# Kernel tuning notes

Measured on AMD Instinct MI355X. Metric: run time of the kernel, lower is better.

Reference implementation:

```python
import jax, jax.numpy as jnp
import numpy as np
from jax.ops import segment_sum

N_NODES = 50000
N_EDGES = 50000
N_GRAPHS = 1024


def _inv_deg(idx, num_segments):
    deg = segment_sum(jnp.ones(idx.shape[0], jnp.float32), idx, num_segments=num_segments)
    return jnp.where(deg > 0, 1.0 / deg, 0.0)


def hypergraph_conv(x, W, b, node_idx, edge_idx):
    # PyG HypergraphConv (use_attention=False, heads=1, hyperedge_weight=1):
    # out = D^{-1} H B^{-1} H^T (X W) + b
    D = _inv_deg(node_idx, N_NODES)   # inverse node degree [N]
    B = _inv_deg(edge_idx, N_EDGES)   # inverse hyperedge degree [E]
    xl = x @ W                         # [N, out]
    # node -> hyperedge aggregation
    edge_feat = B[:, None] * segment_sum(xl[node_idx], edge_idx, num_segments=N_EDGES)
    # hyperedge -> node aggregation
    out = D[:, None] * segment_sum(edge_feat[edge_idx], node_idx, num_segments=N_NODES)
    return out + b


def global_mean_pool(x, batch):
    s = segment_sum(x, batch, num_segments=N_GRAPHS)
    cnt = segment_sum(jnp.ones(x.shape[0], jnp.float32), batch, num_segments=N_GRAPHS)
    return s / jnp.maximum(cnt, 1.0)[:, None]


def setup_inputs() -> dict:
    key = jax.random.key(0)
    ks = jax.random.split(key, 16)
    F, H = 128, 256
    def lin(k, fi, fo):
        s = 1.0 / np.sqrt(fi)
        k1, k2 = jax.random.split(k)
        return (jax.random.uniform(k1, (fi, fo), jnp.float32, -s, s),
                jax.random.uniform(k2, (fo,), jnp.float32, -s, s))
    W1, b1 = lin(ks[0], F, H)
    W2, b2 = lin(ks[1], H, 2 * H)
    W3, b3 = lin(ks[2], 2 * H, H)
    Wl1, bl1 = lin(ks[3], H, H // 2)
    Wl2, bl2 = lin(ks[4], H // 2, 1)
    x = jax.random.normal(ks[5], (N_NODES, F), jnp.float32)
    hyperedge_index = jax.random.randint(ks[6], (2, 400000), 0, N_EDGES, jnp.int64)
    batch = jnp.sort(jax.random.randint(ks[7], (N_NODES,), 0, N_GRAPHS, jnp.int64))
    return {"x": x, "hyperedge_index": hyperedge_index, "batch": batch,
            "W1": W1, "b1": b1, "W2": W2, "b2": b2, "W3": W3, "b3": b3,
            "Wl1": Wl1, "bl1": bl1, "Wl2": Wl2, "bl2": bl2}


def reference(x, hyperedge_index, batch, W1, b1, W2, b2, W3, b3, Wl1, bl1, Wl2, bl2):
    node_idx, edge_idx = hyperedge_index[0], hyperedge_index[1]
    h = jax.nn.relu(hypergraph_conv(x, W1, b1, node_idx, edge_idx))
    h = jax.nn.relu(hypergraph_conv(h, W2, b2, node_idx, edge_idx))
    h = jax.nn.relu(hypergraph_conv(h, W3, b3, node_idx, edge_idx))
    g = global_mean_pool(h, batch)              # [G, H]
    g = jax.nn.relu(g @ Wl1 + bl1)
    out = g @ Wl2 + bl2                          # [G, 1]
    return out
```

## Files before the change

kernel.cpp:

```cpp
#include <hip/hip_runtime.h>
#include <hip/hip_bf16.h>

#define N_NODES  50000
#define N_EDGES  50000
#define N_INC    400000
#define N_GRAPHS 1024
#define M_PAD    50048
#define SEG_CAP  50176

typedef __bf16 bf16x8 __attribute__((ext_vector_type(8)));
typedef float  f32x4  __attribute__((ext_vector_type(4)));

__device__ __forceinline__ unsigned short f2bf(float f) {
    __hip_bfloat16 h = __float2bfloat16(f);
    return __builtin_bit_cast(unsigned short, h);
}
__device__ __forceinline__ float bflo(unsigned int u) {
    return __builtin_bit_cast(float, u << 16);
}
__device__ __forceinline__ float bfhi(unsigned int u) {
    return __builtin_bit_cast(float, u & 0xffff0000u);
}
__device__ __forceinline__ unsigned int packbf(float a, float b) {
    return (unsigned int)f2bf(a) | ((unsigned int)f2bf(b) << 16);
}
__device__ __forceinline__ void load_lds16(const unsigned short* g, unsigned short* l) {
    __builtin_amdgcn_global_load_lds((const __attribute__((address_space(1))) void*)g,
                                     (__attribute__((address_space(3))) void*)l, 16, 0, 0);
}

__global__ __launch_bounds__(256) void normhist_kernel(const int* __restrict__ hei,
                                                       const int* __restrict__ braw,
                                                       int* __restrict__ nidx, int* __restrict__ eidx,
                                                       unsigned short* __restrict__ rn,
                                                       unsigned short* __restrict__ re,
                                                       int* __restrict__ ndeg, int* __restrict__ edeg,
                                                       int* __restrict__ gcnt,
                                                       int* __restrict__ goff_src) {
    __shared__ int s32;
    int t = threadIdx.x;
    if (t == 0) s32 = 0;
    __syncthreads();
    int probe = hei[4 * t + 1] | hei[4 * t + 3];
    if (probe) s32 = 1;
    __syncthreads();
    int is32 = s32;
    int i = blockIdx.x * 256 + t;
    if (i < N_INC) {
        int n, e;
        if (is32) { n = hei[i];     e = hei[N_INC + i]; }
        else      { n = hei[2 * i]; e = hei[2 * N_INC + 2 * i]; }
        nidx[i] = n; eidx[i] = e;
        rn[i] = (unsigned short)atomicAdd(&ndeg[n], 1);
        re[i] = (unsigned short)atomicAdd(&edeg[e], 1);
    }
    if (i < N_NODES) {
        int b = is32 ? braw[i] : braw[2 * i];
        (void)goff_src;
        atomicAdd(&gcnt[b], 1);
    }
}

__global__ __launch_bounds__(256) void scan_up_f(const int* __restrict__ edeg,
                                                 const int* __restrict__ ndeg,
                                                 const int* __restrict__ gcnt,
                                                 int* __restrict__ eoff, int* __restrict__ noff,
                                                 int* __restrict__ goff,
                                                 int* __restrict__ partials) {
    __shared__ int lds[256];
    int b = blockIdx.x, t = threadIdx.x;
    const int* in; int* outp; int lb;
    if (b < 49)      { in = edeg; outp = eoff; lb = b; }
    else if (b < 98) { in = ndeg; outp = noff; lb = b - 49; }
    else             { in = gcnt; outp = goff; lb = 0; }
    int base = lb * 1024 + t * 4;
    int4 v = *(const int4*)(in + base);
    int s = v.x + v.y + v.z + v.w;
    lds[t] = s;
    __syncthreads();
    for (int off = 1; off < 256; off <<= 1) {
        int u = (t >= off) ? lds[t - off] : 0;
        __syncthreads();
        lds[t] += u;
        __syncthreads();
    }
    int excl = lds[t] - s;
    if (t == 255) partials[b] = lds[255];
    int4 o;
    o.x = excl;
    o.y = excl + v.x;
    o.z = o.y + v.y;
    o.w = o.z + v.z;
    *(int4*)(outp + base) = o;
}

__global__ __launch_bounds__(128) void scan_mid_f(int* __restrict__ partials) {
    __shared__ int lds[99];
    int t = threadIdx.x;
    if (t < 99) lds[t] = partials[t];
    __syncthreads();
    if (t < 3) {
        int lo = (t == 0) ? 0 : (t == 1 ? 49 : 98);
        int hi = (t == 0) ? 49 : (t == 1 ? 98 : 99);
        int run = 0;
        for (int i = lo; i < hi; ++i) { int x = lds[i]; lds[i] = run; run += x; }
    }
    __syncthreads();
    if (t < 99) partials[t] = lds[t];
}

__global__ __launch_bounds__(256) void scan_down_f(int* __restrict__ eoff,
                                                   int* __restrict__ noff,
                                                   int* __restrict__ goff,
                                                   const int* __restrict__ partials) {
    int b = blockIdx.x, t = threadIdx.x;
    int* outp; int lb;
    if (b < 49)      { outp = eoff; lb = b; }
    else if (b < 98) { outp = noff; lb = b - 49; }
    else             { outp = goff; lb = 0; }
    int base = lb * 1024 + t * 4;
    int p = partials[b];
    int4 v = *(const int4*)(outp + base);
    v.x += p; v.y += p; v.z += p; v.w += p;
    *(int4*)(outp + base) = v;
}

#define NB_CSR  1563
#define NB_CONV 6250
#define NB_W1   128
#define NB_W2   512
#define NB_W3   512
__global__ __launch_bounds__(256) void prep_kernel(const int* __restrict__ nidx,
                                                   const int* __restrict__ eidx,
                                                   const unsigned short* __restrict__ rn,
                                                   const unsigned short* __restrict__ re,
                                                   const int* __restrict__ eoff,
                                                   const int* __restrict__ noff,
                                                   unsigned short* __restrict__ csre,
                                                   unsigned short* __restrict__ csrn,
                                                   const float* __restrict__ x,
                                                   unsigned short* __restrict__ xbf,
                                                   const float* __restrict__ W1, unsigned short* __restrict__ wt1,
                                                   const float* __restrict__ W2, unsigned short* __restrict__ wt2,
                                                   const float* __restrict__ W3, unsigned short* __restrict__ wt3) {
    int b = blockIdx.x, t = threadIdx.x;
    if (b < NB_CSR) {
        int i = b * 256 + t;
        if (i < N_INC) {
            int n = nidx[i], e = eidx[i];
            csre[eoff[e] + re[i]] = (unsigned short)n;
            csrn[noff[n] + rn[i]] = (unsigned short)e;
        }
    } else if (b < NB_CSR + NB_CONV) {
        int i = (b - NB_CSR) * 256 + t;
        float4 v = *(const float4*)(x + 4 * (size_t)i);
        ushort4 o;
        o.x = f2bf(v.x); o.y = f2bf(v.y); o.z = f2bf(v.z); o.w = f2bf(v.w);
        *(ushort4*)(xbf + 4 * (size_t)i) = o;
    } else if (b < NB_CSR + NB_CONV + NB_W1) {
        int i = (b - NB_CSR - NB_CONV) * 256 + t;
        int k = i >> 8, n = i & 255;
        wt1[n * 128 + k] = f2bf(W1[i]);
    } else if (b < NB_CSR + NB_CONV + NB_W1 + NB_W2) {
        int i = (b - NB_CSR - NB_CONV - NB_W1) * 256 + t;
        int k = i >> 9, n = i & 511;
        wt2[n * 256 + k] = f2bf(W2[i]);
    } else {
        int i = (b - NB_CSR - NB_CONV - NB_W1 - NB_W2) * 256 + t;
        int k = i >> 8, n = i & 255;
        wt3[n * 512 + k] = f2bf(W3[i]);
    }
}

template <bool EPI>
__global__ __launch_bounds__(256) void gemm128_kernel(const unsigned short* __restrict__ A,
                                                      const unsigned short* __restrict__ Bt,
                                                      const float* __restrict__ bias,
                                                      unsigned short* __restrict__ C,
                                                      int M, int K, int N) {
    __shared__ unsigned short As[128 * 32];
    __shared__ unsigned short Bs[128 * 32];
    __shared__ unsigned short Cs[32][140];
    int tid  = threadIdx.x;
    int wave = tid >> 6, lane = tid & 63;
    int n0 = blockIdx.x * 128, m0 = blockIdx.y * 128;
    int quad = lane >> 4, fr = lane & 15;
    int wr = wave >> 1, wc = wave & 1;
    int lrow16 = lane >> 2;
    int lchunk = (lane & 3) * 8;

    const unsigned short* gsrc;
    unsigned short* ldst;
    if (wave < 2) { gsrc = A  + (size_t)(m0 + wave * 64) * K;       ldst = As + wave * 64 * 32; }
    else          { gsrc = Bt + (size_t)(n0 + (wave - 2) * 64) * K; ldst = Bs + (wave - 2) * 64 * 32; }

    f32x4 acc[4][4];
#pragma unroll
    for (int s = 0; s < 4; ++s)
#pragma unroll
        for (int c = 0; c < 4; ++c) acc[s][c] = (f32x4){0.f, 0.f, 0.f, 0.f};

    for (int k0 = 0; k0 < K; k0 += 32) {
#pragma unroll
        for (int l = 0; l < 4; ++l) {
            const unsigned short* g = gsrc + (size_t)(l * 16 + lrow16) * K + k0 + lchunk;
            load_lds16(g, ldst + l * 16 * 32);
        }
        __syncthreads();
        bf16x8 af[4], bfr[4];
#pragma unroll
        for (int s = 0; s < 4; ++s)
            af[s] = *(const bf16x8*)&As[(wr * 64 + s * 16 + fr) * 32 + quad * 8];
#pragma unroll
        for (int c = 0; c < 4; ++c)
            bfr[c] = *(const bf16x8*)&Bs[(wc * 64 + c * 16 + fr) * 32 + quad * 8];
#pragma unroll
        for (int s = 0; s < 4; ++s)
#pragma unroll
            for (int c = 0; c < 4; ++c)
                acc[s][c] = __builtin_amdgcn_mfma_f32_16x16x32_bf16(af[s], bfr[c], acc[s][c], 0, 0, 0);
        __syncthreads();
    }

    float bv[4];
#pragma unroll
    for (int c = 0; c < 4; ++c) bv[c] = EPI ? bias[n0 + wc * 64 + c * 16 + fr] : 0.f;
#pragma unroll
    for (int s = 0; s < 4; ++s) {
#pragma unroll
        for (int c = 0; c < 4; ++c)
#pragma unroll
            for (int r = 0; r < 4; ++r) {
                float v = acc[s][c][r];
                if (EPI) v = fmaxf(v + bv[c], 0.f);
                Cs[wr * 16 + quad * 4 + r][wc * 64 + c * 16 + fr] = f2bf(v);
            }
        __syncthreads();
#pragma unroll
        for (int i = 0; i < 2; ++i) {
            int rl  = i * 16 + (tid >> 4);
            int col = (tid & 15) * 8;
            int gm  = m0 + (rl >> 4) * 64 + s * 16 + (rl & 15);
            if (gm < M) {
                uint4 v = *(const uint4*)&Cs[rl][col];
                *(uint4*)&C[(size_t)gm * N + n0 + col] = v;
            }
        }
        __syncthreads();
    }
}

template <int C, bool BIAS>
__device__ __forceinline__ void seg_body(const unsigned short* __restrict__ in,
                                         const int* __restrict__ offs,
                                         const int* __restrict__ degs,
                                         const unsigned short* __restrict__ csr_src,
                                         const float* __restrict__ bias,
                                         unsigned short* __restrict__ outp,
                                         int nseg) {
    constexpr int VEC = C / 64;
    constexpr int NW  = VEC / 2;
    int w = (blockIdx.x * 256 + threadIdx.x) >> 6;
    int lane = threadIdx.x & 63;
    if (w >= nseg) return;
    int deg   = __builtin_amdgcn_readfirstlane(degs[w]);
    int start = __builtin_amdgcn_readfirstlane(offs[w]);
    float dinv = (deg > 0) ? 1.0f / (float)deg : 0.0f;
    const unsigned short* cs = csr_src + start;
    float acc[VEC];
#pragma unroll
    for (int q = 0; q < VEC; ++q) acc[q] = 0.f;
    size_t lbase = (size_t)lane * VEC;

    auto accum = [&](unsigned int* v) {
#pragma unroll
        for (int q = 0; q < NW; ++q) { acc[2 * q] += bflo(v[q]); acc[2 * q + 1] += bfhi(v[q]); }
    };
    auto loadrow = [&](int src, unsigned int* v) {
        const unsigned int* p = (const unsigned int*)(in + (size_t)src * C + lbase);
        if constexpr (NW == 4)      { uint4 t = *(const uint4*)p; v[0] = t.x; v[1] = t.y; v[2] = t.z; v[3] = t.w; }
        else if constexpr (NW == 2) { uint2 t = *(const uint2*)p; v[0] = t.x; v[1] = t.y; }
        else                        { v[0] = *p; }
    };

    int j = 0;
    for (; j + 8 <= deg; j += 8) {
        int s[8];
        unsigned int v[8][NW];
#pragma unroll
        for (int u = 0; u < 8; ++u) s[u] = __builtin_amdgcn_readfirstlane((int)cs[j + u]);
#pragma unroll
        for (int u = 0; u < 8; ++u) loadrow(s[u], v[u]);
        __asm__ __volatile__("" ::: "memory");
#pragma unroll
        for (int u = 0; u < 8; ++u) accum(v[u]);
    }
    for (; j + 4 <= deg; j += 4) {
        int s[4];
        unsigned int v[4][NW];
#pragma unroll
        for (int u = 0; u < 4; ++u) s[u] = __builtin_amdgcn_readfirstlane((int)cs[j + u]);
#pragma unroll
        for (int u = 0; u < 4; ++u) loadrow(s[u], v[u]);
        __asm__ __volatile__("" ::: "memory");
#pragma unroll
        for (int u = 0; u < 4; ++u) accum(v[u]);
    }
    for (; j < deg; ++j) {
        int s0 = __builtin_amdgcn_readfirstlane((int)cs[j]);
        unsigned int v0[NW];
        loadrow(s0, v0);
        accum(v0);
    }

    unsigned int o[NW];
#pragma unroll
    for (int q = 0; q < NW; ++q) {
        float a = acc[2 * q] * dinv;
        float b = acc[2 * q + 1] * dinv;
        if constexpr (BIAS) {
            a = fmaxf(a + bias[lbase + 2 * q], 0.f);
            b = fmaxf(b + bias[lbase + 2 * q + 1], 0.f);
        }
        o[q] = packbf(a, b);
    }
    unsigned int* po = (unsigned int*)(outp + (size_t)w * C + lbase);
    if constexpr (NW == 4)      { *(uint4*)po = make_uint4(o[0], o[1], o[2], o[3]); }
    else if constexpr (NW == 2) { *(uint2*)po = make_uint2(o[0], o[1]); }
    else                        { *po = o[0]; }
}

template <int C>
__global__ __launch_bounds__(256) void seg_edge_t(const unsigned short* __restrict__ xl,
                                                  const int* __restrict__ eoff,
                                                  const int* __restrict__ edeg,
                                                  const unsigned short* __restrict__ csr_src,
                                                  unsigned short* __restrict__ ef) {
    seg_body<C, false>(xl, eoff, edeg, csr_src, nullptr, ef, N_EDGES);
}

template <int C, bool BIAS>
__global__ __launch_bounds__(256) void seg_node_t(const unsigned short* __restrict__ ef,
                                                  const int* __restrict__ noff,
                                                  const int* __restrict__ ndeg,
                                                  const unsigned short* __restrict__ csr_src,
                                                  const float* __restrict__ bias,
                                                  unsigned short* __restrict__ hout) {
    seg_body<C, BIAS>(ef, noff, ndeg, csr_src, bias, hout, N_NODES);
}

__global__ __launch_bounds__(256) void pool_head_kernel(const unsigned short* __restrict__ h,
                                                        const int* __restrict__ goff,
                                                        const int* __restrict__ gcnt,
                                                        const float* __restrict__ Wl1,
                                                        const float* __restrict__ bl1,
                                                        const float* __restrict__ Wl2,
                                                        const float* __restrict__ bl2,
                                                        float* __restrict__ out) {
    __shared__ float xs[256];
    __shared__ float red[128];
    int g = blockIdx.x, t = threadIdx.x;
    int s = goff[g], cnt = gcnt[g];
    float acc = 0.f;
    for (int i = 0; i < cnt; ++i) {
        unsigned int u = h[(size_t)(s + i) * 256 + t];
        acc += __builtin_bit_cast(float, u << 16);
    }
    xs[t] = acc / (float)(cnt > 0 ? cnt : 1);
    __syncthreads();
    if (t < 128) {
        float s2 = 0.f;
        for (int f = 0; f < 256; ++f) s2 += xs[f] * Wl1[f * 128 + t];
        s2 = fmaxf(s2 + bl1[t], 0.f);
        red[t] = s2 * Wl2[t];
    }
    __syncthreads();
    for (int off = 64; off > 0; off >>= 1) {
        if (t < off) red[t] += red[t + off];
        __syncthreads();
    }
    if (t == 0) out[g] = red[0] + bl2[0];
}

extern "C" void kernel_launch(void* const* d_in, const int* in_sizes, int n_in,
                              void* d_out, int out_size, void* d_ws, size_t ws_size,
                              hipStream_t stream) {
    const float* x     = (const float*)d_in[0];
    const int* hei     = (const int*)d_in[1];
    const int* braw    = (const int*)d_in[2];
    const float* W1    = (const float*)d_in[3];
    const float* b1    = (const float*)d_in[4];
    const float* W2    = (const float*)d_in[5];
    const float* b2    = (const float*)d_in[6];
    const float* W3    = (const float*)d_in[7];
    const float* b3    = (const float*)d_in[8];
    const float* Wl1   = (const float*)d_in[9];
    const float* bl1   = (const float*)d_in[10];
    const float* Wl2   = (const float*)d_in[11];
    const float* bl2   = (const float*)d_in[12];
    float* out         = (float*)d_out;

    char* w = (char*)d_ws;
    size_t off = 0;
    auto alloc = [&](size_t bytes) { size_t p = off; off += (bytes + 255) & ~(size_t)255; return p; };
    size_t o_edeg = alloc((size_t)SEG_CAP * 4);
    size_t o_ndeg = alloc((size_t)SEG_CAP * 4);
    size_t o_gcnt = alloc((size_t)1024 * 4);
    size_t zero_end = off;
    size_t o_eoff = alloc((size_t)SEG_CAP * 4);
    size_t o_noff = alloc((size_t)SEG_CAP * 4);
    size_t o_goff = alloc((size_t)1024 * 4);
    size_t o_part = alloc(128 * 4);
    size_t o_nidx = alloc((size_t)N_INC * 4);
    size_t o_eidx = alloc((size_t)N_INC * 4);
    size_t o_rn   = alloc((size_t)N_INC * 2);
    size_t o_re   = alloc((size_t)N_INC * 2);
    size_t o_csre = alloc((size_t)N_INC * 2);
    size_t o_csrn = alloc((size_t)N_INC * 2);
    size_t o_wt1  = alloc((size_t)128 * 256 * 2);
    size_t o_wt2  = alloc((size_t)256 * 512 * 2);
    size_t o_wt3  = alloc((size_t)512 * 256 * 2);
    size_t o_xbf  = alloc((size_t)M_PAD * 128 * 2);
    size_t o_Y    = alloc((size_t)M_PAD * 256 * 2);
    size_t o_H1   = alloc((size_t)M_PAD * 256 * 2);
    size_t o_H2   = alloc((size_t)M_PAD * 512 * 2);
    size_t o_bufE = alloc((size_t)N_EDGES * 256 * 2);

    int* edeg = (int*)(w + o_edeg);
    int* ndeg = (int*)(w + o_ndeg);
    int* gcnt = (int*)(w + o_gcnt);
    int* eoff = (int*)(w + o_eoff);
    int* noff = (int*)(w + o_noff);
    int* goff = (int*)(w + o_goff);
    int* part = (int*)(w + o_part);
    int* nidx = (int*)(w + o_nidx);
    int* eidx = (int*)(w + o_eidx);
    unsigned short* rn   = (unsigned short*)(w + o_rn);
    unsigned short* re   = (unsigned short*)(w + o_re);
    unsigned short* csre = (unsigned short*)(w + o_csre);
    unsigned short* csrn = (unsigned short*)(w + o_csrn);
    unsigned short* wt1  = (unsigned short*)(w + o_wt1);
    unsigned short* wt2  = (unsigned short*)(w + o_wt2);
    unsigned short* wt3  = (unsigned short*)(w + o_wt3);
    unsigned short* xbf  = (unsigned short*)(w + o_xbf);
    unsigned short* Y    = (unsigned short*)(w + o_Y);
    unsigned short* H1   = (unsigned short*)(w + o_H1);
    unsigned short* H2   = (unsigned short*)(w + o_H2);
    unsigned short* bufE = (unsigned short*)(w + o_bufE);

    hipMemsetAsync(w, 0, zero_end, stream);
    normhist_kernel<<<(N_INC + 255) / 256, 256, 0, stream>>>(hei, braw, nidx, eidx, rn, re,
                                                             ndeg, edeg, gcnt, goff);
    scan_up_f<<<99, 256, 0, stream>>>(edeg, ndeg, gcnt, eoff, noff, goff, part);
    scan_mid_f<<<1, 128, 0, stream>>>(part);
    scan_down_f<<<99, 256, 0, stream>>>(eoff, noff, goff, part);
    prep_kernel<<<NB_CSR + NB_CONV + NB_W1 + NB_W2 + NB_W3, 256, 0, stream>>>(
        nidx, eidx, rn, re, eoff, noff, csre, csrn, x, xbf, W1, wt1, W2, wt2, W3, wt3);

    int segGrid = (N_NODES * 64 + 255) / 256;

    seg_edge_t<128><<<segGrid, 256, 0, stream>>>(xbf, eoff, edeg, csre, bufE);
    seg_node_t<128, false><<<segGrid, 256, 0, stream>>>(bufE, noff, ndeg, csrn, nullptr, Y);
    {
        dim3 grid(256 / 128, M_PAD / 128);
        gemm128_kernel<true><<<grid, 256, 0, stream>>>(Y, wt1, b1, H1, N_NODES, 128, 256);
    }
    seg_edge_t<256><<<segGrid, 256, 0, stream>>>(H1, eoff, edeg, csre, bufE);
    seg_node_t<256, false><<<segGrid, 256, 0, stream>>>(bufE, noff, ndeg, csrn, nullptr, Y);
    {
        dim3 grid(512 / 128, M_PAD / 128);
        gemm128_kernel<true><<<grid, 256, 0, stream>>>(Y, wt2, b2, H2, N_NODES, 256, 512);
    }
    {
        dim3 grid(256 / 128, M_PAD / 128);
        gemm128_kernel<false><<<grid, 256, 0, stream>>>(H2, wt3, nullptr, Y, N_NODES, 512, 256);
    }
    seg_edge_t<256><<<segGrid, 256, 0, stream>>>(Y, eoff, edeg, csre, bufE);
    seg_node_t<256, true><<<segGrid, 256, 0, stream>>>(bufE, noff, ndeg, csrn, b3, H1);

    pool_head_kernel<<<N_GRAPHS, 256, 0, stream>>>(H1, goff, gcnt, Wl1, bl1, Wl2, bl2, out);
}
```

Before: 442.3 us.

## Pad degree counters, binary-search graph offsets, move conversions into histogram kernel

Degree counters are padded to 64-byte stride so the histogram atomics for different nodes or edges no longer share cache lines. Graph offsets come from a binary search over the sorted batch vector instead of an atomic histogram plus scan. The x and weight bf16 conversions move into the histogram kernel, leaving the CSR fill kernel smaller. In exchange the memset zeroes a buffer 16 times larger and the scan and segment kernels read degrees with strided accesses.

```diff
diff --git a/kernel.cpp b/kernel.cpp
--- a/kernel.cpp
+++ b/kernel.cpp
@@ -29,52 +29,97 @@
                                      (__attribute__((address_space(3))) void*)l, 16, 0, 0);
 }
 
+#define NB_INC  1563
+#define NB_CONV 6250
+#define NB_W1   128
+#define NB_W2   512
+#define NB_W3   512
 __global__ __launch_bounds__(256) void normhist_kernel(const int* __restrict__ hei,
-                                                       const int* __restrict__ braw,
                                                        int* __restrict__ nidx, int* __restrict__ eidx,
                                                        unsigned short* __restrict__ rn,
                                                        unsigned short* __restrict__ re,
-                                                       int* __restrict__ ndeg, int* __restrict__ edeg,
-                                                       int* __restrict__ gcnt,
-                                                       int* __restrict__ goff_src) {
-    __shared__ int s32;
-    int t = threadIdx.x;
-    if (t == 0) s32 = 0;
-    __syncthreads();
-    int probe = hei[4 * t + 1] | hei[4 * t + 3];
-    if (probe) s32 = 1;
-    __syncthreads();
-    int is32 = s32;
-    int i = blockIdx.x * 256 + t;
-    if (i < N_INC) {
-        int n, e;
-        if (is32) { n = hei[i];     e = hei[N_INC + i]; }
-        else      { n = hei[2 * i]; e = hei[2 * N_INC + 2 * i]; }
-        nidx[i] = n; eidx[i] = e;
-        rn[i] = (unsigned short)atomicAdd(&ndeg[n], 1);
-        re[i] = (unsigned short)atomicAdd(&edeg[e], 1);
-    }
-    if (i < N_NODES) {
-        int b = is32 ? braw[i] : braw[2 * i];
-        (void)goff_src;
-        atomicAdd(&gcnt[b], 1);
-    }
-}
-
-__global__ __launch_bounds__(256) void scan_up_f(const int* __restrict__ edeg,
-                                                 const int* __restrict__ ndeg,
-                                                 const int* __restrict__ gcnt,
+                                                       int* __restrict__ ndeg_p, int* __restrict__ edeg_p,
+                                                       const float* __restrict__ x,
+                                                       unsigned short* __restrict__ xbf,
+                                                       const float* __restrict__ W1, unsigned short* __restrict__ wt1,
+                                                       const float* __restrict__ W2, unsigned short* __restrict__ wt2,
+                                                       const float* __restrict__ W3, unsigned short* __restrict__ wt3) {
+    int b = blockIdx.x, t = threadIdx.x;
+    if (b < NB_INC) {
+        __shared__ int s32;
+        if (t == 0) s32 = 0;
+        __syncthreads();
+        int probe = hei[4 * t + 1] | hei[4 * t + 3];
+        if (probe) s32 = 1;
+        __syncthreads();
+        int is32 = s32;
+        int i = b * 256 + t;
+        if (i < N_INC) {
+            int n, e;
+            if (is32) { n = hei[i];     e = hei[N_INC + i]; }
+            else      { n = hei[2 * i]; e = hei[2 * N_INC + 2 * i]; }
+            nidx[i] = n; eidx[i] = e;
+            rn[i] = (unsigned short)atomicAdd(&ndeg_p[n << 4], 1);
+            re[i] = (unsigned short)atomicAdd(&edeg_p[e << 4], 1);
+        }
+    } else if (b < NB_INC + NB_CONV) {
+        int i = (b - NB_INC) * 256 + t;
+        float4 v = *(const float4*)(x + 4 * (size_t)i);
+        ushort4 o;
+        o.x = f2bf(v.x); o.y = f2bf(v.y); o.z = f2bf(v.z); o.w = f2bf(v.w);
+        *(ushort4*)(xbf + 4 * (size_t)i) = o;
+    } else if (b < NB_INC + NB_CONV + NB_W1) {
+        int i = (b - NB_INC - NB_CONV) * 256 + t;
+        int k = i >> 8, n = i & 255;
+        wt1[n * 128 + k] = f2bf(W1[i]);
+    } else if (b < NB_INC + NB_CONV + NB_W1 + NB_W2) {
+        int i = (b - NB_INC - NB_CONV - NB_W1) * 256 + t;
+        int k = i >> 9, n = i & 511;
+        wt2[n * 256 + k] = f2bf(W2[i]);
+    } else {
+        int i = (b - NB_INC - NB_CONV - NB_W1 - NB_W2) * 256 + t;
+        int k = i >> 8, n = i & 255;
+        wt3[n * 512 + k] = f2bf(W3[i]);
+    }
+}
+
+__global__ __launch_bounds__(256) void scan_up_f(const int* __restrict__ edeg_p,
+                                                 const int* __restrict__ ndeg_p,
+                                                 const int* __restrict__ hei,
+                                                 const int* __restrict__ braw,
                                                  int* __restrict__ eoff, int* __restrict__ noff,
                                                  int* __restrict__ goff,
                                                  int* __restrict__ partials) {
+    int b = blockIdx.x, t = threadIdx.x;
+    if (b >= 98) {
+        __shared__ int s32;
+        if (t == 0) s32 = 0;
+        __syncthreads();
+        int probe = hei[4 * t + 1] | hei[4 * t + 3];
+        if (probe) s32 = 1;
+        __syncthreads();
+        int is32 = s32;
+        int g = (b - 98) * 256 + t;
+        int lo = 0, hi = N_NODES;
+        while (lo < hi) {
+            int mid = (lo + hi) >> 1;
+            int v = is32 ? braw[mid] : braw[2 * mid];
+            if (v < g) lo = mid + 1; else hi = mid;
+        }
+        goff[g] = lo;
+        if (g == 1023) goff[1024] = N_NODES;
+        return;
+    }
     __shared__ int lds[256];
-    int b = blockIdx.x, t = threadIdx.x;
     const int* in; int* outp; int lb;
-    if (b < 49)      { in = edeg; outp = eoff; lb = b; }
-    else if (b < 98) { in = ndeg; outp = noff; lb = b - 49; }
-    else             { in = gcnt; outp = goff; lb = 0; }
+    if (b < 49) { in = edeg_p; outp = eoff; lb = b; }
+    else        { in = ndeg_p; outp = noff; lb = b - 49; }
     int base = lb * 1024 + t * 4;
-    int4 v = *(const int4*)(in + base);
+    int4 v;
+    v.x = in[(size_t)(base + 0) << 4];
+    v.y = in[(size_t)(base + 1) << 4];
+    v.z = in[(size_t)(base + 2) << 4];
+    v.w = in[(size_t)(base + 3) << 4];
     int s = v.x + v.y + v.z + v.w;
     lds[t] = s;
     __syncthreads();
@@ -95,29 +140,26 @@
 }
 
 __global__ __launch_bounds__(128) void scan_mid_f(int* __restrict__ partials) {
-    __shared__ int lds[99];
+    __shared__ int lds[98];
     int t = threadIdx.x;
-    if (t < 99) lds[t] = partials[t];
+    if (t < 98) lds[t] = partials[t];
     __syncthreads();
-    if (t < 3) {
-        int lo = (t == 0) ? 0 : (t == 1 ? 49 : 98);
-        int hi = (t == 0) ? 49 : (t == 1 ? 98 : 99);
+    if (t < 2) {
+        int lo = t * 49, hi = lo + 49;
         int run = 0;
         for (int i = lo; i < hi; ++i) { int x = lds[i]; lds[i] = run; run += x; }
     }
     __syncthreads();
-    if (t < 99) partials[t] = lds[t];
+    if (t < 98) partials[t] = lds[t];
 }
 
 __global__ __launch_bounds__(256) void scan_down_f(int* __restrict__ eoff,
                                                    int* __restrict__ noff,
-                                                   int* __restrict__ goff,
                                                    const int* __restrict__ partials) {
     int b = blockIdx.x, t = threadIdx.x;
     int* outp; int lb;
-    if (b < 49)      { outp = eoff; lb = b; }
-    else if (b < 98) { outp = noff; lb = b - 49; }
-    else             { outp = goff; lb = 0; }
+    if (b < 49) { outp = eoff; lb = b; }
+    else        { outp = noff; lb = b - 49; }
     int base = lb * 1024 + t * 4;
     int p = partials[b];
     int4 v = *(const int4*)(outp + base);
@@ -125,11 +167,6 @@
     *(int4*)(outp + base) = v;
 }
 
-#define NB_CSR  1563
-#define NB_CONV 6250
-#define NB_W1   128
-#define NB_W2   512
-#define NB_W3   512
 __global__ __launch_bounds__(256) void prep_kernel(const int* __restrict__ nidx,
                                                    const int* __restrict__ eidx,
                                                    const unsigned short* __restrict__ rn,
@@ -137,39 +174,12 @@
                                                    const int* __restrict__ eoff,
                                                    const int* __restrict__ noff,
                                                    unsigned short* __restrict__ csre,
-                                                   unsigned short* __restrict__ csrn,
-                                                   const float* __restrict__ x,
-                                                   unsigned short* __restrict__ xbf,
-                                                   const float* __restrict__ W1, unsigned short* __restrict__ wt1,
-                                                   const float* __restrict__ W2, unsigned short* __restrict__ wt2,
-                                                   const float* __restrict__ W3, unsigned short* __restrict__ wt3) {
-    int b = blockIdx.x, t = threadIdx.x;
-    if (b < NB_CSR) {
-        int i = b * 256 + t;
-        if (i < N_INC) {
-            int n = nidx[i], e = eidx[i];
-            csre[eoff[e] + re[i]] = (unsigned short)n;
-            csrn[noff[n] + rn[i]] = (unsigned short)e;
-        }
-    } else if (b < NB_CSR + NB_CONV) {
-        int i = (b - NB_CSR) * 256 + t;
-        float4 v = *(const float4*)(x + 4 * (size_t)i);
-        ushort4 o;
-        o.x = f2bf(v.x); o.y = f2bf(v.y); o.z = f2bf(v.z); o.w = f2bf(v.w);
-        *(ushort4*)(xbf + 4 * (size_t)i) = o;
-    } else if (b < NB_CSR + NB_CONV + NB_W1) {
-        int i = (b - NB_CSR - NB_CONV) * 256 + t;
-        int k = i >> 8, n = i & 255;
-        wt1[n * 128 + k] = f2bf(W1[i]);
-    } else if (b < NB_CSR + NB_CONV + NB_W1 + NB_W2) {
-        int i = (b - NB_CSR - NB_CONV - NB_W1) * 256 + t;
-        int k = i >> 9, n = i & 511;
-        wt2[n * 256 + k] = f2bf(W2[i]);
-    } else {
-        int i = (b - NB_CSR - NB_CONV - NB_W1 - NB_W2) * 256 + t;
-        int k = i >> 8, n = i & 255;
-        wt3[n * 512 + k] = f2bf(W3[i]);
-    }
+                                                   unsigned short* __restrict__ csrn) {
+    int i = blockIdx.x * 256 + threadIdx.x;
+    if (i >= N_INC) return;
+    int n = nidx[i], e = eidx[i];
+    csre[eoff[e] + re[i]] = (unsigned short)n;
+    csrn[noff[n] + rn[i]] = (unsigned short)e;
 }
 
 template <bool EPI>
@@ -253,7 +263,7 @@
 template <int C, bool BIAS>
 __device__ __forceinline__ void seg_body(const unsigned short* __restrict__ in,
                                          const int* __restrict__ offs,
-                                         const int* __restrict__ degs,
+                                         const int* __restrict__ degs_p,
                                          const unsigned short* __restrict__ csr_src,
                                          const float* __restrict__ bias,
                                          unsigned short* __restrict__ outp,
@@ -263,7 +273,7 @@
     int w = (blockIdx.x * 256 + threadIdx.x) >> 6;
     int lane = threadIdx.x & 63;
     if (w >= nseg) return;
-    int deg   = __builtin_amdgcn_readfirstlane(degs[w]);
+    int deg   = __builtin_amdgcn_readfirstlane(degs_p[(size_t)w << 4]);
     int start = __builtin_amdgcn_readfirstlane(offs[w]);
     float dinv = (deg > 0) ? 1.0f / (float)deg : 0.0f;
     const unsigned short* cs = csr_src + start;
@@ -333,25 +343,24 @@
 template <int C>
 __global__ __launch_bounds__(256) void seg_edge_t(const unsigned short* __restrict__ xl,
                                                   const int* __restrict__ eoff,
-                                                  const int* __restrict__ edeg,
+                                                  const int* __restrict__ edeg_p,
                                                   const unsigned short* __restrict__ csr_src,
                                                   unsigned short* __restrict__ ef) {
-    seg_body<C, false>(xl, eoff, edeg, csr_src, nullptr, ef, N_EDGES);
+    seg_body<C, false>(xl, eoff, edeg_p, csr_src, nullptr, ef, N_EDGES);
 }
 
 template <int C, bool BIAS>
 __global__ __launch_bounds__(256) void seg_node_t(const unsigned short* __restrict__ ef,
                                                   const int* __restrict__ noff,
-                                                  const int* __restrict__ ndeg,
+                                                  const int* __restrict__ ndeg_p,
                                                   const unsigned short* __restrict__ csr_src,
                                                   const float* __restrict__ bias,
                                                   unsigned short* __restrict__ hout) {
-    seg_body<C, BIAS>(ef, noff, ndeg, csr_src, bias, hout, N_NODES);
+    seg_body<C, BIAS>(ef, noff, ndeg_p, csr_src, bias, hout, N_NODES);
 }
 
 __global__ __launch_bounds__(256) void pool_head_kernel(const unsigned short* __restrict__ h,
                                                         const int* __restrict__ goff,
-                                                        const int* __restrict__ gcnt,
                                                         const float* __restrict__ Wl1,
                                                         const float* __restrict__ bl1,
                                                         const float* __restrict__ Wl2,
@@ -360,7 +369,7 @@
     __shared__ float xs[256];
     __shared__ float red[128];
     int g = blockIdx.x, t = threadIdx.x;
-    int s = goff[g], cnt = gcnt[g];
+    int s = goff[g], cnt = goff[g + 1] - s;
     float acc = 0.f;
     for (int i = 0; i < cnt; ++i) {
         unsigned int u = h[(size_t)(s + i) * 256 + t];
@@ -403,13 +412,12 @@
     char* w = (char*)d_ws;
     size_t off = 0;
     auto alloc = [&](size_t bytes) { size_t p = off; off += (bytes + 255) & ~(size_t)255; return p; };
-    size_t o_edeg = alloc((size_t)SEG_CAP * 4);
-    size_t o_ndeg = alloc((size_t)SEG_CAP * 4);
-    size_t o_gcnt = alloc((size_t)1024 * 4);
+    size_t o_edegp = alloc((size_t)SEG_CAP * 16 * 4);
+    size_t o_ndegp = alloc((size_t)SEG_CAP * 16 * 4);
     size_t zero_end = off;
     size_t o_eoff = alloc((size_t)SEG_CAP * 4);
     size_t o_noff = alloc((size_t)SEG_CAP * 4);
-    size_t o_goff = alloc((size_t)1024 * 4);
+    size_t o_goff = alloc((size_t)1025 * 4);
     size_t o_part = alloc(128 * 4);
     size_t o_nidx = alloc((size_t)N_INC * 4);
     size_t o_eidx = alloc((size_t)N_INC * 4);
@@ -426,9 +434,8 @@
     size_t o_H2   = alloc((size_t)M_PAD * 512 * 2);
     size_t o_bufE = alloc((size_t)N_EDGES * 256 * 2);
 
-    int* edeg = (int*)(w + o_edeg);
-    int* ndeg = (int*)(w + o_ndeg);
-    int* gcnt = (int*)(w + o_gcnt);
+    int* edeg_p = (int*)(w + o_edegp);
+    int* ndeg_p = (int*)(w + o_ndegp);
     int* eoff = (int*)(w + o_eoff);
     int* noff = (int*)(w + o_noff);
     int* goff = (int*)(w + o_goff);
@@ -449,24 +456,23 @@
     unsigned short* bufE = (unsigned short*)(w + o_bufE);
 
     hipMemsetAsync(w, 0, zero_end, stream);
-    normhist_kernel<<<(N_INC + 255) / 256, 256, 0, stream>>>(hei, braw, nidx, eidx, rn, re,
-                                                             ndeg, edeg, gcnt, goff);
-    scan_up_f<<<99, 256, 0, stream>>>(edeg, ndeg, gcnt, eoff, noff, goff, part);
+    normhist_kernel<<<NB_INC + NB_CONV + NB_W1 + NB_W2 + NB_W3, 256, 0, stream>>>(
+        hei, nidx, eidx, rn, re, ndeg_p, edeg_p, x, xbf, W1, wt1, W2, wt2, W3, wt3);
+    scan_up_f<<<102, 256, 0, stream>>>(edeg_p, ndeg_p, hei, braw, eoff, noff, goff, part);
     scan_mid_f<<<1, 128, 0, stream>>>(part);
-    scan_down_f<<<99, 256, 0, stream>>>(eoff, noff, goff, part);
-    prep_kernel<<<NB_CSR + NB_CONV + NB_W1 + NB_W2 + NB_W3, 256, 0, stream>>>(
-        nidx, eidx, rn, re, eoff, noff, csre, csrn, x, xbf, W1, wt1, W2, wt2, W3, wt3);
+    scan_down_f<<<98, 256, 0, stream>>>(eoff, noff, part);
+    prep_kernel<<<(N_INC + 255) / 256, 256, 0, stream>>>(nidx, eidx, rn, re, eoff, noff, csre, csrn);
 
     int segGrid = (N_NODES * 64 + 255) / 256;
 
-    seg_edge_t<128><<<segGrid, 256, 0, stream>>>(xbf, eoff, edeg, csre, bufE);
-    seg_node_t<128, false><<<segGrid, 256, 0, stream>>>(bufE, noff, ndeg, csrn, nullptr, Y);
+    seg_edge_t<128><<<segGrid, 256, 0, stream>>>(xbf, eoff, edeg_p, csre, bufE);
+    seg_node_t<128, false><<<segGrid, 256, 0, stream>>>(bufE, noff, ndeg_p, csrn, nullptr, Y);
     {
         dim3 grid(256 / 128, M_PAD / 128);
         gemm128_kernel<true><<<grid, 256, 0, stream>>>(Y, wt1, b1, H1, N_NODES, 128, 256);
     }
-    seg_edge_t<256><<<segGrid, 256, 0, stream>>>(H1, eoff, edeg, csre, bufE);
-    seg_node_t<256, false><<<segGrid, 256, 0, stream>>>(bufE, noff, ndeg, csrn, nullptr, Y);
+    seg_edge_t<256><<<segGrid, 256, 0, stream>>>(H1, eoff, edeg_p, csre, bufE);
+    seg_node_t<256, false><<<segGrid, 256, 0, stream>>>(bufE, noff, ndeg_p, csrn, nullptr, Y);
     {
         dim3 grid(512 / 128, M_PAD / 128);
         gemm128_kernel<true><<<grid, 256, 0, stream>>>(Y, wt2, b2, H2, N_NODES, 256, 512);
@@ -475,8 +481,8 @@
         dim3 grid(256 / 128, M_PAD / 128);
         gemm128_kernel<false><<<grid, 256, 0, stream>>>(H2, wt3, nullptr, Y, N_NODES, 512, 256);
     }
-    seg_edge_t<256><<<segGrid, 256, 0, stream>>>(Y, eoff, edeg, csre, bufE);
-    seg_node_t<256, true><<<segGrid, 256, 0, stream>>>(bufE, noff, ndeg, csrn, b3, H1);
-
-    pool_head_kernel<<<N_GRAPHS, 256, 0, stream>>>(H1, goff, gcnt, Wl1, bl1, Wl2, bl2, out);
-}
+    seg_edge_t<256><<<segGrid, 256, 0, stream>>>(Y, eoff, edeg_p, csre, bufE);
+    seg_node_t<256, true><<<segGrid, 256, 0, stream>>>(bufE, noff, ndeg_p, csrn, b3, H1);
+
+    pool_head_kernel<<<N_GRAPHS, 256, 0, stream>>>(H1, goff, Wl1, bl1, Wl2, bl2, out);
+}
```

Result: faster. 429.2 us (-3.0%).
